# Kernel optimization log

Measured on AMD Instinct MI355X. Metric: run time of the kernel, lower is better.

The kernel has to match this reference:

```python
import jax, jax.numpy as jnp
import numpy as np

N, M, A, B, L, C = 40000, 12, 64, 64, 3, 128  # atoms, nbrs, site feat, bond feat, layers, crystals
F0, H = 92, 128  # orig site features, hidden dim
EPS = 1e-5


def _bn(x, g, b):
    # BatchNorm1d in training mode: batch stats (biased var), affine
    m = x.mean(0)
    v = x.var(0)
    return g * (x - m) * jax.lax.rsqrt(v + EPS) + b


def setup_inputs() -> dict:
    key = jax.random.key(0)
    ks = jax.random.split(key, 20)
    inp = {
        "site_features": jax.random.normal(ks[0], (N, F0), jnp.float32),
        "bond_features": jax.random.normal(ks[1], (N, M, B), jnp.float32),
        "feature_after_pooing": jax.random.normal(ks[2], (C,), jnp.float32),
        "fc1_w": jax.random.normal(ks[3], (F0, A), jnp.float32) * 0.05,
        "fc1_b": jnp.zeros((A,), jnp.float32),
        "conv_fc_w": jax.random.normal(ks[4], (L, 2 * A + B, 2 * A), jnp.float32) * 0.05,
        "conv_fc_b": jnp.zeros((L, 2 * A), jnp.float32),
        "bn1_g": jnp.ones((L, 2 * A), jnp.float32),
        "bn1_b": jnp.zeros((L, 2 * A), jnp.float32),
        "bn2_g": jnp.ones((L, A), jnp.float32),
        "bn2_b": jnp.zeros((L, A), jnp.float32),
        "top_bn_g": jnp.ones((A + 1,), jnp.float32),
        "top_bn_b": jnp.zeros((A + 1,), jnp.float32),
        "fc2_w": jax.random.normal(ks[5], (A + 1, H), jnp.float32) * 0.05,
        "fc2_b": jnp.zeros((H,), jnp.float32),
        "fc3_w": jax.random.normal(ks[6], (H, 1), jnp.float32) * 0.05,
        "fc3_b": jnp.zeros((1,), jnp.float32),
        "bond_indices": jax.random.randint(ks[7], (N, M), 0, N, jnp.int64),
        "crystal_idx": jnp.sort(jax.random.randint(ks[8], (N,), 0, C, jnp.int64)),
    }
    return inp


def _conv_layer(h, bond_features, bond_indices, w, bw, g1, b1, g2, b2):
    n, a = h.shape
    m = bond_indices.shape[1]
    v_j = h[bond_indices]                                 # (N,M,A) gather
    v_i = jnp.broadcast_to(h[:, None, :], (n, m, a))      # (N,M,A)
    z = jnp.concatenate([v_i, v_j, bond_features], -1)    # (N,M,2A+B)
    t = jnp.einsum('nmk,kd->nmd', z, w) + bw              # (N,M,2A)
    t = _bn(t.reshape(-1, 2 * a), g1, b1).reshape(n, m, 2 * a)
    filt, core = t[..., :a], t[..., a:]
    s = jnp.sum(jax.nn.sigmoid(filt) * jax.nn.softplus(core), axis=1)  # (N,A)
    s = _bn(s, g2, b2)
    return jax.nn.softplus(h + s)


def reference(site_features, bond_features, feature_after_pooing,
              fc1_w, fc1_b, conv_fc_w, conv_fc_b, bn1_g, bn1_b, bn2_g, bn2_b,
              top_bn_g, top_bn_b, fc2_w, fc2_b, fc3_w, fc3_b,
              bond_indices, crystal_idx):
    h = site_features @ fc1_w + fc1_b  # (N,A)
    for l in range(L):
        h = _conv_layer(h, bond_features, bond_indices,
                        conv_fc_w[l], conv_fc_b[l],
                        bn1_g[l], bn1_b[l], bn2_g[l], bn2_b[l])
    # per-crystal mean pooling
    counts = jax.ops.segment_sum(jnp.ones((N,), h.dtype), crystal_idx, num_segments=C)
    pooled = jax.ops.segment_sum(h, crystal_idx, num_segments=C) / jnp.maximum(counts, 1.0)[:, None]
    feats = jnp.concatenate([pooled, feature_after_pooing[:, None]], axis=1)  # (C,A+1)
    feats = _bn(feats, top_bn_g, top_bn_b)
    hidden = jax.nn.softplus(feats) @ fc2_w + fc2_b
    pred = jax.nn.softplus(hidden) @ fc3_w + fc3_b
    return pred.reshape(-1)
```

## Files before the change

### kernel.cpp

```cpp
#include <hip/hip_runtime.h>
#include <hip/hip_bf16.h>


#define NN 40000
#define MM 12
#define AA 64
#define LL 3
#define CC 128
#define F0C 92
#define NBOND (NN*MM)
#define EPSBN 1e-5f

#define G_BOND 1250
#define NTILE 7500
#define G_FUSE 1250
#define NSUPER 2500
#define RED_B 125

#define L2E 1.4426950408889634f
#define LN2 0.6931471805599453f

typedef __attribute__((ext_vector_type(8))) short bf16x8;
typedef __attribute__((ext_vector_type(4))) float f32x4;

__device__ __forceinline__ float softplusf_(float x) {
    float e = __builtin_amdgcn_exp2f(-fabsf(x) * L2E);
    return fmaxf(x, 0.f) + __builtin_amdgcn_logf(1.f + e) * LN2;
}
__device__ __forceinline__ float sigmoidf_(float x) {
    return __builtin_amdgcn_rcpf(1.f + __builtin_amdgcn_exp2f(-x * L2E));
}
__device__ __forceinline__ unsigned short f2bf(float f) {
    unsigned int u = __float_as_uint(f);
    unsigned int r = (u + 0x7fffu + ((u >> 16) & 1u)) >> 16;
    return (unsigned short)r;
}
__device__ __forceinline__ float bf2f(unsigned short s) {
    return __uint_as_float(((unsigned int)s) << 16);
}

__global__ __launch_bounds__(256) void k_cvt(const float* __restrict__ in,
        unsigned short* __restrict__ out) {
    size_t i = ((size_t)blockIdx.x * 256 + threadIdx.x) * 8;
    float4 a = *(const float4*)&in[i];
    float4 b = *(const float4*)&in[i + 4];
    ushort4 ua, ub;
    ua.x = f2bf(a.x); ua.y = f2bf(a.y); ua.z = f2bf(a.z); ua.w = f2bf(a.w);
    ub.x = f2bf(b.x); ub.y = f2bf(b.y); ub.z = f2bf(b.z); ub.w = f2bf(b.w);
    *(ushort4*)&out[i] = ua;
    *(ushort4*)&out[i + 4] = ub;
}

__global__ __launch_bounds__(256) void k_fc1(const float* __restrict__ site,
        const float* __restrict__ w, const float* __restrict__ b,
        float* __restrict__ h) {
    __shared__ float w_s[F0C][AA];
    __shared__ float x_s[16][F0C];
    int tid = threadIdx.x;
    for (int i = tid; i < F0C * AA; i += 256) w_s[i / AA][i % AA] = w[i];
    int n0 = blockIdx.x * 16;
    for (int i = tid; i < 16 * F0C; i += 256) x_s[i / F0C][i % F0C] = site[(size_t)n0 * F0C + i];
    __syncthreads();
    int d = tid & 63, ng = tid >> 6;
    float bb = b[d];
    float acc[4] = {bb, bb, bb, bb};
    #pragma unroll 4
    for (int k = 0; k < F0C; ++k) {
        float wv = w_s[k][d];
        acc[0] += x_s[ng][k] * wv;
        acc[1] += x_s[ng + 4][k] * wv;
        acc[2] += x_s[ng + 8][k] * wv;
        acc[3] += x_s[ng + 12][k] * wv;
    }
    #pragma unroll
    for (int rr = 0; rr < 4; ++rr)
        h[(size_t)(n0 + ng + rr * 4) * AA + d] = acc[rr];
}

__global__ __launch_bounds__(256) void k_proj(const float* __restrict__ h,
        const float* __restrict__ convw, const float* __restrict__ convb,
        unsigned short* __restrict__ hi, unsigned short* __restrict__ hj) {
    __shared__ float w_s[64][256];
    __shared__ float hT[64][36];
    int tid = threadIdx.x;
    for (int i = tid; i < 64 * 256; i += 256) {
        int k = i >> 8, c = i & 255;
        w_s[k][c] = convw[(size_t)((c < 128 ? k : 64 + k)) * 128 + (c & 127)];
    }
    int row0 = blockIdx.x * 32;
    for (int i = tid; i < 2048; i += 256) {
        int r = i >> 6, k = i & 63;
        hT[k][r] = h[(size_t)(row0 + r) * 64 + k];
    }
    __syncthreads();
    int c0 = (tid & 63) * 4;
    int r0 = (tid >> 6) * 8;
    float acc[8][4];
    #pragma unroll
    for (int r = 0; r < 8; ++r)
        #pragma unroll
        for (int i = 0; i < 4; ++i) acc[r][i] = 0.f;
    #pragma unroll 4
    for (int k = 0; k < 64; ++k) {
        float4 w4 = *(const float4*)&w_s[k][c0];
        float4 ha = *(const float4*)&hT[k][r0];
        float4 hb = *(const float4*)&hT[k][r0 + 4];
        float wv[4] = {w4.x, w4.y, w4.z, w4.w};
        float hv[8] = {ha.x, ha.y, ha.z, ha.w, hb.x, hb.y, hb.z, hb.w};
        #pragma unroll
        for (int r = 0; r < 8; ++r)
            #pragma unroll
            for (int i = 0; i < 4; ++i) acc[r][i] += hv[r] * wv[i];
    }
    bool isHi = (c0 < 128);
    int cc = isHi ? c0 : c0 - 128;
    float4 cb4 = make_float4(0.f, 0.f, 0.f, 0.f);
    if (isHi) cb4 = *(const float4*)&convb[c0];
    unsigned short* dst = isHi ? hi : hj;
    #pragma unroll
    for (int r = 0; r < 8; ++r) {
        int n = row0 + r0 + r;
        ushort4 o;
        o.x = f2bf(acc[r][0] + cb4.x);
        o.y = f2bf(acc[r][1] + cb4.y);
        o.z = f2bf(acc[r][2] + cb4.z);
        o.w = f2bf(acc[r][3] + cb4.w);
        *(ushort4*)&dst[(size_t)n * 128 + cc] = o;
    }
}

template<bool BFQ>
__global__ __launch_bounds__(256) void k_stat(const float* __restrict__ bf,
        const unsigned short* __restrict__ bfq,
        const float* __restrict__ wb,
        const unsigned short* __restrict__ hi, const unsigned short* __restrict__ hj,
        const int* __restrict__ bidx,
        float* __restrict__ part1) {
    __shared__ __align__(16) char buf0[128 * 72 * 2];
    __shared__ __align__(16) char buf1[64 * 72 * 2];
    auto wbT   = (unsigned short(*)[72])buf0;
    auto red   = (float(*)[128])buf0;
    auto A_lds = (unsigned short(*)[72])buf1;

    int tid = threadIdx.x;
    int lane = tid & 63, w = tid >> 6;
    int l15 = lane & 15, l4 = lane >> 4;

    for (int i = tid; i < 64 * 128; i += 256) {
        int k = i >> 7, c = i & 127;
        wbT[c][k] = f2bf(wb[i]);
    }
    __syncthreads();

    bf16x8 bfr[2][8];
    #pragma unroll
    for (int kh = 0; kh < 2; ++kh)
        #pragma unroll
        for (int ct = 0; ct < 8; ++ct)
            bfr[kh][ct] = *(const bf16x8*)&wbT[ct * 16 + l15][kh * 32 + l4 * 8];

    float suml[8], sql[8];
    #pragma unroll
    for (int ct = 0; ct < 8; ++ct) { suml[ct] = 0.f; sql[ct] = 0.f; }

    int rbase = w * 16 + l4 * 4;
    for (int tile = blockIdx.x; tile < NTILE; tile += G_BOND) {
        int bond0 = tile * 64;
        __syncthreads();
        if constexpr (BFQ) {
            int r = tid >> 3, c8 = (tid & 7) * 8;
            #pragma unroll
            for (int rr = 0; rr < 2; ++rr) {
                bf16x8 v = *(const bf16x8*)&bfq[((size_t)(bond0 + r + rr * 32)) * 64 + c8];
                *(bf16x8*)&A_lds[r + rr * 32][c8] = v;
            }
        } else {
            int r = tid >> 4, kq = (tid & 15) * 4;
            #pragma unroll
            for (int rr = 0; rr < 4; ++rr) {
                float4 v = *(const float4*)&bf[((size_t)(bond0 + r + rr * 16)) * 64 + kq];
                ushort4 u;
                u.x = f2bf(v.x); u.y = f2bf(v.y); u.z = f2bf(v.z); u.w = f2bf(v.w);
                *(ushort4*)&A_lds[r + rr * 16][kq] = u;
            }
        }
        __syncthreads();

        f32x4 acc[8];
        #pragma unroll
        for (int ct = 0; ct < 8; ++ct) acc[ct] = (f32x4){0.f, 0.f, 0.f, 0.f};
        #pragma unroll
        for (int kh = 0; kh < 2; ++kh) {
            bf16x8 a = *(const bf16x8*)&A_lds[rbase - l4 * 4 + l15][kh * 32 + l4 * 8];
            #pragma unroll
            for (int ct = 0; ct < 8; ++ct)
                acc[ct] = __builtin_amdgcn_mfma_f32_16x16x32_bf16(a, bfr[kh][ct], acc[ct], 0, 0, 0);
        }

        #pragma unroll
        for (int reg = 0; reg < 4; ++reg) {
            int bond = bond0 + rbase + reg;
            int n = bond / MM;
            int j = bidx[bond];
            const unsigned short* hin = hi + (size_t)n * 128;
            const unsigned short* hjn = hj + (size_t)j * 128;
            #pragma unroll
            for (int ct = 0; ct < 8; ++ct) {
                int col = ct * 16 + l15;
                float t = acc[ct][reg] + bf2f(hin[col]) + bf2f(hjn[col]);
                suml[ct] += t;
                sql[ct] += t * t;
            }
        }
    }

    #pragma unroll
    for (int ct = 0; ct < 8; ++ct) {
        float s = suml[ct], q = sql[ct];
        s += __shfl_xor(s, 16); s += __shfl_xor(s, 32);
        q += __shfl_xor(q, 16); q += __shfl_xor(q, 32);
        suml[ct] = s; sql[ct] = q;
    }
    __syncthreads();
    if (l4 == 0) {
        #pragma unroll
        for (int ct = 0; ct < 8; ++ct) red[w][ct * 16 + l15] = suml[ct];
    }
    __syncthreads();
    if (tid < 128)
        part1[(size_t)blockIdx.x * 256 + tid] = red[0][tid] + red[1][tid] + red[2][tid] + red[3][tid];
    __syncthreads();
    if (l4 == 0) {
        #pragma unroll
        for (int ct = 0; ct < 8; ++ct) red[w][ct * 16 + l15] = sql[ct];
    }
    __syncthreads();
    if (tid < 128)
        part1[(size_t)blockIdx.x * 256 + 128 + tid] = red[0][tid] + red[1][tid] + red[2][tid] + red[3][tid];
}

template<bool BFQ>
__global__ __launch_bounds__(256) void k_fuse(const float* __restrict__ bf,
        const unsigned short* __restrict__ bfq,
        const float* __restrict__ wb,
        const unsigned short* __restrict__ hi, const unsigned short* __restrict__ hj,
        const int* __restrict__ bidx,
        const float* __restrict__ scsh,
        float* __restrict__ s_out,
        float* __restrict__ part2) {
    __shared__ __align__(16) char buf0[192 * 68 * 2];
    __shared__ __align__(16) char buf1[64 * 72 * 2];
    auto wbT   = (unsigned short(*)[72])buf0;
    auto val   = (unsigned short(*)[68])buf0;
    auto A_lds = (unsigned short(*)[72])buf1;
    auto red2  = (float(*)[64])buf1;

    int tid = threadIdx.x;
    int lane = tid & 63, w = tid >> 6;
    int l15 = lane & 15, l4 = lane >> 4;

    for (int i = tid; i < 64 * 128; i += 256) {
        int k = i >> 7, c = i & 127;
        wbT[c][k] = f2bf(wb[i]);
    }
    __syncthreads();

    bf16x8 bfr[2][8];
    #pragma unroll
    for (int kh = 0; kh < 2; ++kh)
        #pragma unroll
        for (int ct = 0; ct < 8; ++ct)
            bfr[kh][ct] = *(const bf16x8*)&wbT[ct * 16 + l15][kh * 32 + l4 * 8];

    float scf[4], shf[4], scc[4], shc[4];
    #pragma unroll
    for (int ct = 0; ct < 4; ++ct) {
        int colA = ct * 16 + l15, colC = colA + 64;
        scf[ct] = scsh[colA];  shf[ct] = scsh[128 + colA];
        scc[ct] = scsh[colC];  shc[ct] = scsh[128 + colC];
    }

    int ssite = tid >> 4, a0 = (tid & 15) * 4;
    float sum2[4] = {0, 0, 0, 0}, sq2[4] = {0, 0, 0, 0};

    int rbase = w * 16 + l4 * 4;
    for (int sup = blockIdx.x; sup < NSUPER; sup += G_FUSE) {
        int bond00 = sup * 192;
        #pragma unroll
        for (int sub = 0; sub < 3; ++sub) {
            int bond0 = bond00 + sub * 64;
            __syncthreads();
            if constexpr (BFQ) {
                int r = tid >> 3, c8 = (tid & 7) * 8;
                #pragma unroll
                for (int rr = 0; rr < 2; ++rr) {
                    bf16x8 v = *(const bf16x8*)&bfq[((size_t)(bond0 + r + rr * 32)) * 64 + c8];
                    *(bf16x8*)&A_lds[r + rr * 32][c8] = v;
                }
            } else {
                int r = tid >> 4, kq = (tid & 15) * 4;
                #pragma unroll
                for (int rr = 0; rr < 4; ++rr) {
                    float4 v = *(const float4*)&bf[((size_t)(bond0 + r + rr * 16)) * 64 + kq];
                    ushort4 u;
                    u.x = f2bf(v.x); u.y = f2bf(v.y); u.z = f2bf(v.z); u.w = f2bf(v.w);
                    *(ushort4*)&A_lds[r + rr * 16][kq] = u;
                }
            }
            __syncthreads();

            f32x4 acc[8];
            #pragma unroll
            for (int ct = 0; ct < 8; ++ct) acc[ct] = (f32x4){0.f, 0.f, 0.f, 0.f};
            #pragma unroll
            for (int kh = 0; kh < 2; ++kh) {
                bf16x8 a = *(const bf16x8*)&A_lds[w * 16 + l15][kh * 32 + l4 * 8];
                #pragma unroll
                for (int ct = 0; ct < 8; ++ct)
                    acc[ct] = __builtin_amdgcn_mfma_f32_16x16x32_bf16(a, bfr[kh][ct], acc[ct], 0, 0, 0);
            }

            #pragma unroll
            for (int reg = 0; reg < 4; ++reg) {
                int r = rbase + reg;
                int bond = bond0 + r;
                int n = bond / MM;
                int j = bidx[bond];
                const unsigned short* hin = hi + (size_t)n * 128;
                const unsigned short* hjn = hj + (size_t)j * 128;
                #pragma unroll
                for (int ct = 0; ct < 4; ++ct) {
                    int colA = ct * 16 + l15, colC = colA + 64;
                    float tA = acc[ct][reg]     + bf2f(hin[colA]) + bf2f(hjn[colA]);
                    float tC = acc[ct + 4][reg] + bf2f(hin[colC]) + bf2f(hjn[colC]);
                    float v = sigmoidf_(scf[ct] * tA + shf[ct])
                            * softplusf_(scc[ct] * tC + shc[ct]);
                    val[sub * 64 + r][colA] = f2bf(v);
                }
            }
        }
        __syncthreads();

        float sv[4] = {0, 0, 0, 0};
        #pragma unroll
        for (int m = 0; m < MM; ++m) {
            ushort4 u = *(const ushort4*)&val[ssite * MM + m][a0];
            sv[0] += bf2f(u.x); sv[1] += bf2f(u.y);
            sv[2] += bf2f(u.z); sv[3] += bf2f(u.w);
        }
        int gsite = sup * 16 + ssite;
        *(float4*)&s_out[(size_t)gsite * 64 + a0] = make_float4(sv[0], sv[1], sv[2], sv[3]);
        #pragma unroll
        for (int k = 0; k < 4; ++k) { sum2[k] += sv[k]; sq2[k] += sv[k] * sv[k]; }
    }

    __syncthreads();
    #pragma unroll
    for (int k = 0; k < 4; ++k) red2[ssite][a0 + k] = sum2[k];
    __syncthreads();
    if (tid < 64) {
        float t = 0.f;
        #pragma unroll
        for (int g = 0; g < 16; ++g) t += red2[g][tid];
        part2[(size_t)blockIdx.x * 128 + tid] = t;
    }
    __syncthreads();
    #pragma unroll
    for (int k = 0; k < 4; ++k) red2[ssite][a0 + k] = sq2[k];
    __syncthreads();
    if (tid < 64) {
        float t = 0.f;
        #pragma unroll
        for (int g = 0; g < 16; ++g) t += red2[g][tid];
        part2[(size_t)blockIdx.x * 128 + 64 + tid] = t;
    }
}

__global__ __launch_bounds__(256) void k_red1(const float* __restrict__ in, float* __restrict__ out) {
    int tid = threadIdx.x, b = blockIdx.x;
    float acc = 0.f;
    for (int r = b * 10; r < b * 10 + 10; ++r) acc += in[(size_t)r * 256 + tid];
    out[(size_t)b * 256 + tid] = acc;
}
__global__ __launch_bounds__(128) void k_red2(const float* __restrict__ in, float* __restrict__ out) {
    int tid = threadIdx.x, b = blockIdx.x;
    float acc = 0.f;
    for (int r = b * 10; r < b * 10 + 10; ++r) acc += in[(size_t)r * 128 + tid];
    out[(size_t)b * 128 + tid] = acc;
}

__global__ __launch_bounds__(256) void k_fin1(const float* __restrict__ partA, const float* __restrict__ g,
                       const float* __restrict__ b, float* __restrict__ scsh) {
    __shared__ float sm[256];
    int tid = threadIdx.x;
    float acc = 0.f;
    for (int r = 0; r < RED_B; ++r) acc += partA[(size_t)r * 256 + tid];
    sm[tid] = acc;
    __syncthreads();
    if (tid < 128) {
        float m = sm[tid] / (float)NBOND;
        float v = sm[128 + tid] / (float)NBOND - m * m;
        float sc = g[tid] * rsqrtf(v + EPSBN);
        scsh[tid] = sc;
        scsh[128 + tid] = b[tid] - m * sc;
    }
}

__global__ __launch_bounds__(128) void k_fin2(const float* __restrict__ partB, const float* __restrict__ g,
                       const float* __restrict__ b, float* __restrict__ scsh2) {
    __shared__ float sm[128];
    int tid = threadIdx.x;
    float acc = 0.f;
    for (int r = 0; r < RED_B; ++r) acc += partB[(size_t)r * 128 + tid];
    sm[tid] = acc;
    __syncthreads();
    if (tid < 64) {
        float m = sm[tid] / (float)NN;
        float v = sm[64 + tid] / (float)NN - m * m;
        float sc = g[tid] * rsqrtf(v + EPSBN);
        scsh2[tid] = sc;
        scsh2[64 + tid] = b[tid] - m * sc;
    }
}

__global__ __launch_bounds__(256) void k_upd(float* __restrict__ h, const float* __restrict__ s,
        const float* __restrict__ scsh2) {
    size_t i = ((size_t)blockIdx.x * 256 + threadIdx.x) * 4;
    int c0 = (int)(i & 63);
    float4 hv = *(const float4*)&h[i];
    float4 sv = *(const float4*)&s[i];
    float4 o;
    o.x = softplusf_(hv.x + scsh2[c0 + 0] * sv.x + scsh2[64 + c0 + 0]);
    o.y = softplusf_(hv.y + scsh2[c0 + 1] * sv.y + scsh2[64 + c0 + 1]);
    o.z = softplusf_(hv.z + scsh2[c0 + 2] * sv.z + scsh2[64 + c0 + 2]);
    o.w = softplusf_(hv.w + scsh2[c0 + 3] * sv.w + scsh2[64 + c0 + 3]);
    *(float4*)&h[i] = o;
}

__device__ __forceinline__ int lbound(const int* a, int n, int v) {
    int lo = 0, hi = n;
    while (lo < hi) { int mid = (lo + hi) >> 1; if (a[mid] < v) lo = mid + 1; else hi = mid; }
    return lo;
}

__global__ __launch_bounds__(256) void k_pool(const float* __restrict__ h,
        const int* __restrict__ cidx, float* __restrict__ feats) {
    __shared__ float red[4][68];
    __shared__ int bounds[2];
    int c = blockIdx.x, tid = threadIdx.x;
    if (tid == 0) {
        bounds[0] = lbound(cidx, NN, c);
        bounds[1] = lbound(cidx, NN, c + 1);
    }
    __syncthreads();
    int lo = bounds[0], hi = bounds[1];
    int d = tid & 63, g = tid >> 6;
    float acc = 0;
    for (int n = lo + g; n < hi; n += 4) acc += h[(size_t)n * 64 + d];
    red[g][d] = acc;
    __syncthreads();
    if (tid < 64) {
        float t = red[0][tid] + red[1][tid] + red[2][tid] + red[3][tid];
        int cnt = hi - lo;
        feats[(size_t)c * 65 + tid] = t / (float)(cnt > 0 ? cnt : 1);
    }
}

__global__ __launch_bounds__(128) void k_head1(float* __restrict__ feats, const float* __restrict__ fap,
        const float* __restrict__ g, const float* __restrict__ b, float* __restrict__ featsp) {
    int tid = threadIdx.x;
    if (tid < CC) feats[(size_t)tid * 65 + 64] = fap[tid];
    __syncthreads();
    if (tid < 65) {
        float s = 0;
        for (int r = 0; r < CC; ++r) s += feats[r * 65 + tid];
        float m = s / (float)CC;
        float v = 0;
        for (int r = 0; r < CC; ++r) { float d = feats[r * 65 + tid] - m; v += d * d; }
        v /= (float)CC;
        float sc = g[tid] * rsqrtf(v + EPSBN);
        float sh = b[tid] - m * sc;
        for (int r = 0; r < CC; ++r)
            featsp[r * 65 + tid] = softplusf_(sc * feats[r * 65 + tid] + sh);
    }
}

__global__ __launch_bounds__(128) void k_head2(const float* __restrict__ featsp,
        const float* __restrict__ fc2w, const float* __restrict__ fc2b,
        const float* __restrict__ fc3w, const float* __restrict__ fc3b,
        float* __restrict__ out) {
    __shared__ float fr[65];
    __shared__ float red[128];
    int r = blockIdx.x, tid = threadIdx.x;
    if (tid < 65) fr[tid] = featsp[(size_t)r * 65 + tid];
    __syncthreads();
    float acc = fc2b[tid];
    for (int k = 0; k < 65; ++k) acc += fr[k] * fc2w[k * 128 + tid];
    red[tid] = softplusf_(acc) * fc3w[tid];
    __syncthreads();
    for (int st = 64; st > 0; st >>= 1) {
        if (tid < st) red[tid] += red[tid + st];
        __syncthreads();
    }
    if (tid == 0) out[r] = red[0] + fc3b[0];
}

extern "C" void kernel_launch(void* const* d_in, const int* in_sizes, int n_in,
                              void* d_out, int out_size, void* d_ws, size_t ws_size,
                              hipStream_t stream) {
    const float* site  = (const float*)d_in[0];
    const float* bondf = (const float*)d_in[1];
    const float* fap   = (const float*)d_in[2];
    const float* fc1w  = (const float*)d_in[3];
    const float* fc1b  = (const float*)d_in[4];
    const float* convw = (const float*)d_in[5];
    const float* convb = (const float*)d_in[6];
    const float* bn1g  = (const float*)d_in[7];
    const float* bn1b  = (const float*)d_in[8];
    const float* bn2g  = (const float*)d_in[9];
    const float* bn2b  = (const float*)d_in[10];
    const float* topg  = (const float*)d_in[11];
    const float* topb  = (const float*)d_in[12];
    const float* fc2w  = (const float*)d_in[13];
    const float* fc2b  = (const float*)d_in[14];
    const float* fc3w  = (const float*)d_in[15];
    const float* fc3b  = (const float*)d_in[16];
    const int*   bidx  = (const int*)d_in[17];
    const int*   cidx  = (const int*)d_in[18];
    float* out = (float*)d_out;

    char* w = (char*)d_ws;
    constexpr size_t SZ_H  = (size_t)NN * 64 * 4;
    constexpr size_t SZ_HP = (size_t)NN * 128 * 2;
    constexpr size_t OFF_H  = 0;
    constexpr size_t OFF_HI = OFF_H + SZ_H;
    constexpr size_t OFF_HJ = OFF_HI + SZ_HP;
    constexpr size_t OFF_S  = OFF_HJ + SZ_HP;
    constexpr size_t OFF_SCSH1 = OFF_S + SZ_H;
    constexpr size_t OFF_SCSH2 = OFF_SCSH1 + 1024;
    constexpr size_t OFF_P1 = OFF_SCSH2 + 512;
    constexpr size_t OFF_P2 = OFF_P1 + (size_t)G_BOND * 256 * 4;
    constexpr size_t OFF_PA = OFF_P2 + (size_t)G_FUSE * 128 * 4;
    constexpr size_t OFF_PB = OFF_PA + (size_t)RED_B * 256 * 4;
    constexpr size_t OFF_FE = OFF_PB + (size_t)RED_B * 128 * 4;
    constexpr size_t OFF_FP = OFF_FE + 128 * 65 * 4;
    constexpr size_t OFF_BFQ = ((OFF_FP + 128 * 65 * 4) + 255) & ~(size_t)255;
    constexpr size_t NEED_BFQ = OFF_BFQ + (size_t)NBOND * 64 * 2;

    float* h      = (float*)(w + OFF_H);
    unsigned short* hi = (unsigned short*)(w + OFF_HI);
    unsigned short* hj = (unsigned short*)(w + OFF_HJ);
    float* sbuf   = (float*)(w + OFF_S);
    float* scsh1  = (float*)(w + OFF_SCSH1);
    float* scsh2  = (float*)(w + OFF_SCSH2);
    float* part1  = (float*)(w + OFF_P1);
    float* part2  = (float*)(w + OFF_P2);
    float* partA  = (float*)(w + OFF_PA);
    float* partB  = (float*)(w + OFF_PB);
    float* feats  = (float*)(w + OFF_FE);
    float* featsp = (float*)(w + OFF_FP);
    unsigned short* bfq = (unsigned short*)(w + OFF_BFQ);

    const bool useq = (ws_size >= NEED_BFQ);

    if (useq) k_cvt<<<NBOND * 64 / (256 * 8), 256, 0, stream>>>(bondf, bfq);
    k_fc1<<<2500, 256, 0, stream>>>(site, fc1w, fc1b, h);
    for (int l = 0; l < LL; ++l) {
        const float* cw = convw + (size_t)l * 192 * 128;
        const float* cb = convb + l * 128;
        k_proj<<<1250, 256, 0, stream>>>(h, cw, cb, hi, hj);
        if (useq) {
            k_stat<true><<<G_BOND, 256, 0, stream>>>(bondf, bfq, cw + 128 * 128, hi, hj, bidx, part1);
        } else {
            k_stat<false><<<G_BOND, 256, 0, stream>>>(bondf, bfq, cw + 128 * 128, hi, hj, bidx, part1);
        }
        k_red1<<<RED_B, 256, 0, stream>>>(part1, partA);
        k_fin1<<<1, 256, 0, stream>>>(partA, bn1g + l * 128, bn1b + l * 128, scsh1);
        if (useq) {
            k_fuse<true><<<G_FUSE, 256, 0, stream>>>(bondf, bfq, cw + 128 * 128, hi, hj, bidx, scsh1, sbuf, part2);
        } else {
            k_fuse<false><<<G_FUSE, 256, 0, stream>>>(bondf, bfq, cw + 128 * 128, hi, hj, bidx, scsh1, sbuf, part2);
        }
        k_red2<<<RED_B, 128, 0, stream>>>(part2, partB);
        k_fin2<<<1, 128, 0, stream>>>(partB, bn2g + l * 64, bn2b + l * 64, scsh2);
        k_upd<<<2500, 256, 0, stream>>>(h, sbuf, scsh2);
    }
    k_pool<<<128, 256, 0, stream>>>(h, cidx, feats);
    k_head1<<<1, 128, 0, stream>>>(feats, fap, topg, topb, featsp);
    k_head2<<<128, 128, 0, stream>>>(featsp, fc2w, fc2b, fc3w, fc3b, out);
}
```

Before: 557.8 us.

## Compute BN1 mean analytically via neighbor counts and bond-feature column sums

The first BatchNorm mean is now derived algebraically. It combines per-column sums of the projected hi/hj (hj weighted by how often each atom appears as a neighbor) with a one-time column sum of bond features multiplied by the bond weights. The stat pass therefore only accumulates sums of squares. k_stat and k_fuse now read weight fragments straight from LDS with swapped MFMA operands, and they use vectorized hi/hj loads per lane. Grid and tile sizes also change: 1024 blocks, and k_fuse runs 48-bond tiles with 192 threads. Added costs are a neighbor-count atomic pass, extra reductions in k_proj, and a possible precision loss from computing variance as E[x²]−mean² with an externally computed mean.

New measurement: 816.4 us. +46.4%, slower.

```diff
diff --git a/kernel.cpp b/kernel.cpp
--- a/kernel.cpp
+++ b/kernel.cpp
@@ -11,11 +11,11 @@
 #define NBOND (NN*MM)
 #define EPSBN 1e-5f
 
-#define G_BOND 1250
-#define NTILE 7500
-#define G_FUSE 1250
-#define NSUPER 2500
-#define RED_B 125
+#define G_STAT 1024
+#define NT_STAT 7500
+#define G_FUSE 1024
+#define NT_FUSE 10000
+#define G_PROJ 1250
 
 #define L2E 1.4426950408889634f
 #define LN2 0.6931471805599453f
@@ -51,6 +51,40 @@
     *(ushort4*)&out[i + 4] = ub;
 }
 
+__global__ __launch_bounds__(256) void k_zero(int* __restrict__ cnt) {
+    int i = blockIdx.x * 256 + threadIdx.x;
+    if (i < NN) cnt[i] = 0;
+}
+__global__ __launch_bounds__(256) void k_cnt(const int* __restrict__ bidx,
+        int* __restrict__ cnt) {
+    int i = blockIdx.x * 256 + threadIdx.x;
+    if (i < NBOND) atomicAdd(&cnt[bidx[i]], 1);
+}
+
+template<bool BFQ>
+__global__ __launch_bounds__(256) void k_sbf(const float* __restrict__ bf,
+        const unsigned short* __restrict__ bfq, float* __restrict__ part) {
+    __shared__ float red[4][64];
+    int tid = threadIdx.x, c = tid & 63, rg = tid >> 6;
+    size_t base = (size_t)blockIdx.x * 1875;
+    float acc = 0.f;
+    for (int r = rg; r < 1875; r += 4) {
+        if constexpr (BFQ) acc += bf2f(bfq[(base + r) * 64 + c]);
+        else               acc += bf2f(f2bf(bf[(base + r) * 64 + c]));
+    }
+    red[rg][c] = acc;
+    __syncthreads();
+    if (tid < 64) part[(size_t)blockIdx.x * 64 + tid]
+        = red[0][tid] + red[1][tid] + red[2][tid] + red[3][tid];
+}
+__global__ __launch_bounds__(64) void k_sbf2(const float* __restrict__ part,
+        float* __restrict__ sbf) {
+    int tid = threadIdx.x;
+    float a = 0.f;
+    for (int b = 0; b < 256; ++b) a += part[(size_t)b * 64 + tid];
+    sbf[tid] = a;
+}
+
 __global__ __launch_bounds__(256) void k_fc1(const float* __restrict__ site,
         const float* __restrict__ w, const float* __restrict__ b,
         float* __restrict__ h) {
@@ -79,7 +113,9 @@
 
 __global__ __launch_bounds__(256) void k_proj(const float* __restrict__ h,
         const float* __restrict__ convw, const float* __restrict__ convb,
-        unsigned short* __restrict__ hi, unsigned short* __restrict__ hj) {
+        const int* __restrict__ cnt,
+        unsigned short* __restrict__ hi, unsigned short* __restrict__ hj,
+        float* __restrict__ partP) {
     __shared__ float w_s[64][256];
     __shared__ float hT[64][36];
     int tid = threadIdx.x;
@@ -117,6 +153,7 @@
     float4 cb4 = make_float4(0.f, 0.f, 0.f, 0.f);
     if (isHi) cb4 = *(const float4*)&convb[c0];
     unsigned short* dst = isHi ? hi : hj;
+    float psum[4] = {0.f, 0.f, 0.f, 0.f};
     #pragma unroll
     for (int r = 0; r < 8; ++r) {
         int n = row0 + r0 + r;
@@ -126,7 +163,20 @@
         o.z = f2bf(acc[r][2] + cb4.z);
         o.w = f2bf(acc[r][3] + cb4.w);
         *(ushort4*)&dst[(size_t)n * 128 + cc] = o;
-    }
+        float wt = isHi ? 1.f : (float)cnt[n];
+        psum[0] += wt * bf2f(o.x);
+        psum[1] += wt * bf2f(o.y);
+        psum[2] += wt * bf2f(o.z);
+        psum[3] += wt * bf2f(o.w);
+    }
+    __syncthreads();
+    float* redp = &w_s[0][0];
+    int rg = tid >> 6;
+    #pragma unroll
+    for (int i = 0; i < 4; ++i) redp[rg * 256 + c0 + i] = psum[i];
+    __syncthreads();
+    partP[(size_t)blockIdx.x * 256 + tid] =
+        redp[tid] + redp[256 + tid] + redp[512 + tid] + redp[768 + tid];
 }
 
 template<bool BFQ>
@@ -135,12 +185,10 @@
         const float* __restrict__ wb,
         const unsigned short* __restrict__ hi, const unsigned short* __restrict__ hj,
         const int* __restrict__ bidx,
-        float* __restrict__ part1) {
-    __shared__ __align__(16) char buf0[128 * 72 * 2];
-    __shared__ __align__(16) char buf1[64 * 72 * 2];
-    auto wbT   = (unsigned short(*)[72])buf0;
-    auto red   = (float(*)[128])buf0;
-    auto A_lds = (unsigned short(*)[72])buf1;
+        float* __restrict__ partS) {
+    __shared__ unsigned short wbT[128][72];
+    __shared__ unsigned short A_lds[64][72];
+    __shared__ float red[4][128];
 
     int tid = threadIdx.x;
     int lane = tid & 63, w = tid >> 6;
@@ -150,97 +198,125 @@
         int k = i >> 7, c = i & 127;
         wbT[c][k] = f2bf(wb[i]);
     }
-    __syncthreads();
-
-    bf16x8 bfr[2][8];
+
+    float sql[8][4];
     #pragma unroll
-    for (int kh = 0; kh < 2; ++kh)
-        #pragma unroll
-        for (int ct = 0; ct < 8; ++ct)
-            bfr[kh][ct] = *(const bf16x8*)&wbT[ct * 16 + l15][kh * 32 + l4 * 8];
-
-    float suml[8], sql[8];
-    #pragma unroll
-    for (int ct = 0; ct < 8; ++ct) { suml[ct] = 0.f; sql[ct] = 0.f; }
-
-    int rbase = w * 16 + l4 * 4;
-    for (int tile = blockIdx.x; tile < NTILE; tile += G_BOND) {
+    for (int ct = 0; ct < 8; ++ct)
+        #pragma unroll
+        for (int r = 0; r < 4; ++r) sql[ct][r] = 0.f;
+
+    int myb = w * 16 + l15;
+    for (int tile = blockIdx.x; tile < NT_STAT; tile += G_STAT) {
         int bond0 = tile * 64;
         __syncthreads();
-        if constexpr (BFQ) {
-            int r = tid >> 3, c8 = (tid & 7) * 8;
-            #pragma unroll
-            for (int rr = 0; rr < 2; ++rr) {
-                bf16x8 v = *(const bf16x8*)&bfq[((size_t)(bond0 + r + rr * 32)) * 64 + c8];
-                *(bf16x8*)&A_lds[r + rr * 32][c8] = v;
+        #pragma unroll
+        for (int ii = 0; ii < 2; ++ii) {
+            int idx = tid + ii * 256;
+            int r = idx >> 3, k8 = (idx & 7) * 8;
+            if constexpr (BFQ) {
+                bf16x8 v = *(const bf16x8*)&bfq[((size_t)(bond0 + r)) * 64 + k8];
+                *(bf16x8*)&A_lds[r][k8] = v;
+            } else {
+                float4 v0 = *(const float4*)&bf[((size_t)(bond0 + r)) * 64 + k8];
+                float4 v1 = *(const float4*)&bf[((size_t)(bond0 + r)) * 64 + k8 + 4];
+                ushort4 ua, ub;
+                ua.x = f2bf(v0.x); ua.y = f2bf(v0.y); ua.z = f2bf(v0.z); ua.w = f2bf(v0.w);
+                ub.x = f2bf(v1.x); ub.y = f2bf(v1.y); ub.z = f2bf(v1.z); ub.w = f2bf(v1.w);
+                *(ushort4*)&A_lds[r][k8] = ua;
+                *(ushort4*)&A_lds[r][k8 + 4] = ub;
             }
-        } else {
-            int r = tid >> 4, kq = (tid & 15) * 4;
-            #pragma unroll
-            for (int rr = 0; rr < 4; ++rr) {
-                float4 v = *(const float4*)&bf[((size_t)(bond0 + r + rr * 16)) * 64 + kq];
-                ushort4 u;
-                u.x = f2bf(v.x); u.y = f2bf(v.y); u.z = f2bf(v.z); u.w = f2bf(v.w);
-                *(ushort4*)&A_lds[r + rr * 16][kq] = u;
+        }
+        __syncthreads();
+
+        f32x4 acc[8];
+        #pragma unroll
+        for (int ct = 0; ct < 8; ++ct) acc[ct] = (f32x4){0.f, 0.f, 0.f, 0.f};
+        #pragma unroll
+        for (int kh = 0; kh < 2; ++kh) {
+            bf16x8 a = *(const bf16x8*)&A_lds[myb][kh * 32 + l4 * 8];
+            #pragma unroll
+            for (int ct = 0; ct < 8; ++ct) {
+                bf16x8 wf = *(const bf16x8*)&wbT[ct * 16 + l15][kh * 32 + l4 * 8];
+                acc[ct] = __builtin_amdgcn_mfma_f32_16x16x32_bf16(wf, a, acc[ct], 0, 0, 0);
             }
         }
-        __syncthreads();
-
-        f32x4 acc[8];
-        #pragma unroll
-        for (int ct = 0; ct < 8; ++ct) acc[ct] = (f32x4){0.f, 0.f, 0.f, 0.f};
-        #pragma unroll
-        for (int kh = 0; kh < 2; ++kh) {
-            bf16x8 a = *(const bf16x8*)&A_lds[rbase - l4 * 4 + l15][kh * 32 + l4 * 8];
-            #pragma unroll
-            for (int ct = 0; ct < 8; ++ct)
-                acc[ct] = __builtin_amdgcn_mfma_f32_16x16x32_bf16(a, bfr[kh][ct], acc[ct], 0, 0, 0);
-        }
-
-        #pragma unroll
-        for (int reg = 0; reg < 4; ++reg) {
-            int bond = bond0 + rbase + reg;
-            int n = bond / MM;
-            int j = bidx[bond];
-            const unsigned short* hin = hi + (size_t)n * 128;
-            const unsigned short* hjn = hj + (size_t)j * 128;
-            #pragma unroll
-            for (int ct = 0; ct < 8; ++ct) {
-                int col = ct * 16 + l15;
-                float t = acc[ct][reg] + bf2f(hin[col]) + bf2f(hjn[col]);
-                suml[ct] += t;
-                sql[ct] += t * t;
+
+        int bond = bond0 + myb;
+        int n = bond / MM;
+        int j = bidx[bond];
+        const unsigned short* hin = hi + (size_t)n * 128;
+        const unsigned short* hjn = hj + (size_t)j * 128;
+        #pragma unroll
+        for (int ct = 0; ct < 8; ++ct) {
+            int c0 = ct * 16 + l4 * 4;
+            ushort4 h4 = *(const ushort4*)&hin[c0];
+            ushort4 j4 = *(const ushort4*)&hjn[c0];
+            float hh[4] = {bf2f(h4.x), bf2f(h4.y), bf2f(h4.z), bf2f(h4.w)};
+            float jj[4] = {bf2f(j4.x), bf2f(j4.y), bf2f(j4.z), bf2f(j4.w)};
+            #pragma unroll
+            for (int r = 0; r < 4; ++r) {
+                float t = acc[ct][r] + hh[r] + jj[r];
+                sql[ct][r] += t * t;
             }
         }
     }
 
     #pragma unroll
-    for (int ct = 0; ct < 8; ++ct) {
-        float s = suml[ct], q = sql[ct];
-        s += __shfl_xor(s, 16); s += __shfl_xor(s, 32);
-        q += __shfl_xor(q, 16); q += __shfl_xor(q, 32);
-        suml[ct] = s; sql[ct] = q;
-    }
-    __syncthreads();
-    if (l4 == 0) {
-        #pragma unroll
-        for (int ct = 0; ct < 8; ++ct) red[w][ct * 16 + l15] = suml[ct];
+    for (int ct = 0; ct < 8; ++ct)
+        #pragma unroll
+        for (int r = 0; r < 4; ++r) {
+            float q = sql[ct][r];
+            q += __shfl_xor(q, 1); q += __shfl_xor(q, 2);
+            q += __shfl_xor(q, 4); q += __shfl_xor(q, 8);
+            sql[ct][r] = q;
+        }
+    if (l15 == 0) {
+        #pragma unroll
+        for (int ct = 0; ct < 8; ++ct)
+            #pragma unroll
+            for (int r = 0; r < 4; ++r)
+                red[w][ct * 16 + l4 * 4 + r] = sql[ct][r];
     }
     __syncthreads();
     if (tid < 128)
-        part1[(size_t)blockIdx.x * 256 + tid] = red[0][tid] + red[1][tid] + red[2][tid] + red[3][tid];
-    __syncthreads();
-    if (l4 == 0) {
-        #pragma unroll
-        for (int ct = 0; ct < 8; ++ct) red[w][ct * 16 + l15] = sql[ct];
-    }
-    __syncthreads();
-    if (tid < 128)
-        part1[(size_t)blockIdx.x * 256 + 128 + tid] = red[0][tid] + red[1][tid] + red[2][tid] + red[3][tid];
+        partS[(size_t)blockIdx.x * 128 + tid] =
+            red[0][tid] + red[1][tid] + red[2][tid] + red[3][tid];
+}
+
+__global__ void k_redw(const float* __restrict__ in, float* __restrict__ out,
+                       int rows, int rper) {
+    int tid = threadIdx.x, b = blockIdx.x, W = blockDim.x;
+    float a = 0.f;
+    int r0 = b * rper, r1 = r0 + rper;
+    for (int r = r0; r < r1 && r < rows; ++r) a += in[(size_t)r * W + tid];
+    out[(size_t)b * W + tid] = a;
+}
+
+__global__ __launch_bounds__(128) void k_fin1(const float* __restrict__ partSA,
+        const float* __restrict__ partPA,
+        const float* __restrict__ sbf,
+        const float* __restrict__ wb,
+        const float* __restrict__ g, const float* __restrict__ b,
+        float* __restrict__ scsh) {
+    int c = threadIdx.x;
+    float sq = 0.f;
+    for (int r = 0; r < 128; ++r) sq += partSA[(size_t)r * 128 + c];
+    float his = 0.f, hjw = 0.f;
+    for (int r = 0; r < 125; ++r) {
+        his += partPA[(size_t)r * 256 + c];
+        hjw += partPA[(size_t)r * 256 + 128 + c];
+    }
+    float sw = 0.f;
+    for (int k = 0; k < 64; ++k) sw += sbf[k] * bf2f(f2bf(wb[(size_t)k * 128 + c]));
+    float mean = (sw + 12.f * his + hjw) * (1.f / (float)NBOND);
+    float var = sq * (1.f / (float)NBOND) - mean * mean;
+    float sc = g[c] * rsqrtf(var + EPSBN);
+    scsh[c] = sc;
+    scsh[128 + c] = b[c] - mean * sc;
 }
 
 template<bool BFQ>
-__global__ __launch_bounds__(256) void k_fuse(const float* __restrict__ bf,
+__global__ __launch_bounds__(192) void k_fuse(const float* __restrict__ bf,
         const unsigned short* __restrict__ bfq,
         const float* __restrict__ wb,
         const unsigned short* __restrict__ hi, const unsigned short* __restrict__ hj,
@@ -248,170 +324,145 @@
         const float* __restrict__ scsh,
         float* __restrict__ s_out,
         float* __restrict__ part2) {
-    __shared__ __align__(16) char buf0[192 * 68 * 2];
-    __shared__ __align__(16) char buf1[64 * 72 * 2];
-    auto wbT   = (unsigned short(*)[72])buf0;
-    auto val   = (unsigned short(*)[68])buf0;
-    auto A_lds = (unsigned short(*)[72])buf1;
-    auto red2  = (float(*)[64])buf1;
+    __shared__ unsigned short wbT[128][72];
+    __shared__ unsigned short A_lds[48][72];
+    __shared__ unsigned short val[48][68];
+    __shared__ float red2[4][64];
 
     int tid = threadIdx.x;
     int lane = tid & 63, w = tid >> 6;
     int l15 = lane & 15, l4 = lane >> 4;
 
-    for (int i = tid; i < 64 * 128; i += 256) {
+    for (int i = tid; i < 64 * 128; i += 192) {
         int k = i >> 7, c = i & 127;
         wbT[c][k] = f2bf(wb[i]);
     }
-    __syncthreads();
-
-    bf16x8 bfr[2][8];
+
+    float scf[4][4], shf[4][4], scc[4][4], shc[4][4];
     #pragma unroll
-    for (int kh = 0; kh < 2; ++kh)
-        #pragma unroll
-        for (int ct = 0; ct < 8; ++ct)
-            bfr[kh][ct] = *(const bf16x8*)&wbT[ct * 16 + l15][kh * 32 + l4 * 8];
-
-    float scf[4], shf[4], scc[4], shc[4];
-    #pragma unroll
-    for (int ct = 0; ct < 4; ++ct) {
-        int colA = ct * 16 + l15, colC = colA + 64;
-        scf[ct] = scsh[colA];  shf[ct] = scsh[128 + colA];
-        scc[ct] = scsh[colC];  shc[ct] = scsh[128 + colC];
-    }
-
-    int ssite = tid >> 4, a0 = (tid & 15) * 4;
+    for (int ct = 0; ct < 4; ++ct)
+        #pragma unroll
+        for (int r = 0; r < 4; ++r) {
+            int cf = ct * 16 + l4 * 4 + r;
+            scf[ct][r] = scsh[cf];       shf[ct][r] = scsh[128 + cf];
+            scc[ct][r] = scsh[64 + cf];  shc[ct][r] = scsh[192 + cf];
+        }
+
     float sum2[4] = {0, 0, 0, 0}, sq2[4] = {0, 0, 0, 0};
-
-    int rbase = w * 16 + l4 * 4;
-    for (int sup = blockIdx.x; sup < NSUPER; sup += G_FUSE) {
-        int bond00 = sup * 192;
-        #pragma unroll
-        for (int sub = 0; sub < 3; ++sub) {
-            int bond0 = bond00 + sub * 64;
-            __syncthreads();
+    int myb = w * 16 + l15;
+    __syncthreads();
+
+    for (int tile = blockIdx.x; tile < NT_FUSE; tile += G_FUSE) {
+        int bond0 = tile * 48;
+        #pragma unroll
+        for (int ii = 0; ii < 2; ++ii) {
+            int idx = tid + ii * 192;
+            int r = idx >> 3, k8 = (idx & 7) * 8;
             if constexpr (BFQ) {
-                int r = tid >> 3, c8 = (tid & 7) * 8;
-                #pragma unroll
-                for (int rr = 0; rr < 2; ++rr) {
-                    bf16x8 v = *(const bf16x8*)&bfq[((size_t)(bond0 + r + rr * 32)) * 64 + c8];
-                    *(bf16x8*)&A_lds[r + rr * 32][c8] = v;
-                }
+                bf16x8 v = *(const bf16x8*)&bfq[((size_t)(bond0 + r)) * 64 + k8];
+                *(bf16x8*)&A_lds[r][k8] = v;
             } else {
-                int r = tid >> 4, kq = (tid & 15) * 4;
-                #pragma unroll
-                for (int rr = 0; rr < 4; ++rr) {
-                    float4 v = *(const float4*)&bf[((size_t)(bond0 + r + rr * 16)) * 64 + kq];
-                    ushort4 u;
-                    u.x = f2bf(v.x); u.y = f2bf(v.y); u.z = f2bf(v.z); u.w = f2bf(v.w);
-                    *(ushort4*)&A_lds[r + rr * 16][kq] = u;
-                }
+                float4 v0 = *(const float4*)&bf[((size_t)(bond0 + r)) * 64 + k8];
+                float4 v1 = *(const float4*)&bf[((size_t)(bond0 + r)) * 64 + k8 + 4];
+                ushort4 ua, ub;
+                ua.x = f2bf(v0.x); ua.y = f2bf(v0.y); ua.z = f2bf(v0.z); ua.w = f2bf(v0.w);
+                ub.x = f2bf(v1.x); ub.y = f2bf(v1.y); ub.z = f2bf(v1.z); ub.w = f2bf(v1.w);
+                *(ushort4*)&A_lds[r][k8] = ua;
+                *(ushort4*)&A_lds[r][k8 + 4] = ub;
             }
-            __syncthreads();
-
-            f32x4 acc[8];
-            #pragma unroll
-            for (int ct = 0; ct < 8; ++ct) acc[ct] = (f32x4){0.f, 0.f, 0.f, 0.f};
-            #pragma unroll
-            for (int kh = 0; kh < 2; ++kh) {
-                bf16x8 a = *(const bf16x8*)&A_lds[w * 16 + l15][kh * 32 + l4 * 8];
-                #pragma unroll
-                for (int ct = 0; ct < 8; ++ct)
-                    acc[ct] = __builtin_amdgcn_mfma_f32_16x16x32_bf16(a, bfr[kh][ct], acc[ct], 0, 0, 0);
+        }
+        __syncthreads();
+
+        f32x4 acc[8];
+        #pragma unroll
+        for (int ct = 0; ct < 8; ++ct) acc[ct] = (f32x4){0.f, 0.f, 0.f, 0.f};
+        #pragma unroll
+        for (int kh = 0; kh < 2; ++kh) {
+            bf16x8 a = *(const bf16x8*)&A_lds[myb][kh * 32 + l4 * 8];
+            #pragma unroll
+            for (int ct = 0; ct < 8; ++ct) {
+                bf16x8 wf = *(const bf16x8*)&wbT[ct * 16 + l15][kh * 32 + l4 * 8];
+                acc[ct] = __builtin_amdgcn_mfma_f32_16x16x32_bf16(wf, a, acc[ct], 0, 0, 0);
             }
-
-            #pragma unroll
-            for (int reg = 0; reg < 4; ++reg) {
-                int r = rbase + reg;
-                int bond = bond0 + r;
-                int n = bond / MM;
-                int j = bidx[bond];
-                const unsigned short* hin = hi + (size_t)n * 128;
-                const unsigned short* hjn = hj + (size_t)j * 128;
-                #pragma unroll
-                for (int ct = 0; ct < 4; ++ct) {
-                    int colA = ct * 16 + l15, colC = colA + 64;
-                    float tA = acc[ct][reg]     + bf2f(hin[colA]) + bf2f(hjn[colA]);
-                    float tC = acc[ct + 4][reg] + bf2f(hin[colC]) + bf2f(hjn[colC]);
-                    float v = sigmoidf_(scf[ct] * tA + shf[ct])
-                            * softplusf_(scc[ct] * tC + shc[ct]);
-                    val[sub * 64 + r][colA] = f2bf(v);
-                }
+        }
+
+        int bond = bond0 + myb;
+        int n = bond / MM;
+        int j = bidx[bond];
+        const unsigned short* hin = hi + (size_t)n * 128;
+        const unsigned short* hjn = hj + (size_t)j * 128;
+        #pragma unroll
+        for (int ct = 0; ct < 4; ++ct) {
+            int c0 = ct * 16 + l4 * 4;
+            ushort4 hf = *(const ushort4*)&hin[c0];
+            ushort4 jf = *(const ushort4*)&hjn[c0];
+            ushort4 hc = *(const ushort4*)&hin[c0 + 64];
+            ushort4 jc = *(const ushort4*)&hjn[c0 + 64];
+            float hfv[4] = {bf2f(hf.x), bf2f(hf.y), bf2f(hf.z), bf2f(hf.w)};
+            float jfv[4] = {bf2f(jf.x), bf2f(jf.y), bf2f(jf.z), bf2f(jf.w)};
+            float hcv[4] = {bf2f(hc.x), bf2f(hc.y), bf2f(hc.z), bf2f(hc.w)};
+            float jcv[4] = {bf2f(jc.x), bf2f(jc.y), bf2f(jc.z), bf2f(jc.w)};
+            ushort4 o;
+            unsigned short ov[4];
+            #pragma unroll
+            for (int r = 0; r < 4; ++r) {
+                float tA = acc[ct][r] + hfv[r] + jfv[r];
+                float tC = acc[ct + 4][r] + hcv[r] + jcv[r];
+                float v = sigmoidf_(scf[ct][r] * tA + shf[ct][r])
+                        * softplusf_(scc[ct][r] * tC + shc[ct][r]);
+                ov[r] = f2bf(v);
             }
+            o.x = ov[0]; o.y = ov[1]; o.z = ov[2]; o.w = ov[3];
+            *(ushort4*)&val[myb][c0] = o;
         }
         __syncthreads();
 
-        float sv[4] = {0, 0, 0, 0};
-        #pragma unroll
-        for (int m = 0; m < MM; ++m) {
-            ushort4 u = *(const ushort4*)&val[ssite * MM + m][a0];
-            sv[0] += bf2f(u.x); sv[1] += bf2f(u.y);
-            sv[2] += bf2f(u.z); sv[3] += bf2f(u.w);
-        }
-        int gsite = sup * 16 + ssite;
-        *(float4*)&s_out[(size_t)gsite * 64 + a0] = make_float4(sv[0], sv[1], sv[2], sv[3]);
-        #pragma unroll
-        for (int k = 0; k < 4; ++k) { sum2[k] += sv[k]; sq2[k] += sv[k] * sv[k]; }
-    }
-
-    __syncthreads();
-    #pragma unroll
-    for (int k = 0; k < 4; ++k) red2[ssite][a0 + k] = sum2[k];
-    __syncthreads();
+        if (tid < 64) {
+            int site = tid >> 4, q = tid & 15;
+            float sv[4] = {0, 0, 0, 0};
+            #pragma unroll
+            for (int m = 0; m < MM; ++m) {
+                ushort4 u = *(const ushort4*)&val[site * MM + m][q * 4];
+                sv[0] += bf2f(u.x); sv[1] += bf2f(u.y);
+                sv[2] += bf2f(u.z); sv[3] += bf2f(u.w);
+            }
+            int gsite = tile * 4 + site;
+            *(float4*)&s_out[(size_t)gsite * 64 + q * 4] =
+                make_float4(sv[0], sv[1], sv[2], sv[3]);
+            #pragma unroll
+            for (int i = 0; i < 4; ++i) { sum2[i] += sv[i]; sq2[i] += sv[i] * sv[i]; }
+        }
+        __syncthreads();
+    }
+
     if (tid < 64) {
-        float t = 0.f;
-        #pragma unroll
-        for (int g = 0; g < 16; ++g) t += red2[g][tid];
-        part2[(size_t)blockIdx.x * 128 + tid] = t;
-    }
-    __syncthreads();
-    #pragma unroll
-    for (int k = 0; k < 4; ++k) red2[ssite][a0 + k] = sq2[k];
+        int site = tid >> 4, q = tid & 15;
+        #pragma unroll
+        for (int i = 0; i < 4; ++i) red2[site][q * 4 + i] = sum2[i];
+    }
+    __syncthreads();
+    if (tid < 64)
+        part2[(size_t)blockIdx.x * 128 + tid] =
+            red2[0][tid] + red2[1][tid] + red2[2][tid] + red2[3][tid];
     __syncthreads();
     if (tid < 64) {
-        float t = 0.f;
-        #pragma unroll
-        for (int g = 0; g < 16; ++g) t += red2[g][tid];
-        part2[(size_t)blockIdx.x * 128 + 64 + tid] = t;
-    }
-}
-
-__global__ __launch_bounds__(256) void k_red1(const float* __restrict__ in, float* __restrict__ out) {
-    int tid = threadIdx.x, b = blockIdx.x;
-    float acc = 0.f;
-    for (int r = b * 10; r < b * 10 + 10; ++r) acc += in[(size_t)r * 256 + tid];
-    out[(size_t)b * 256 + tid] = acc;
-}
-__global__ __launch_bounds__(128) void k_red2(const float* __restrict__ in, float* __restrict__ out) {
-    int tid = threadIdx.x, b = blockIdx.x;
-    float acc = 0.f;
-    for (int r = b * 10; r < b * 10 + 10; ++r) acc += in[(size_t)r * 128 + tid];
-    out[(size_t)b * 128 + tid] = acc;
-}
-
-__global__ __launch_bounds__(256) void k_fin1(const float* __restrict__ partA, const float* __restrict__ g,
-                       const float* __restrict__ b, float* __restrict__ scsh) {
-    __shared__ float sm[256];
-    int tid = threadIdx.x;
-    float acc = 0.f;
-    for (int r = 0; r < RED_B; ++r) acc += partA[(size_t)r * 256 + tid];
-    sm[tid] = acc;
-    __syncthreads();
-    if (tid < 128) {
-        float m = sm[tid] / (float)NBOND;
-        float v = sm[128 + tid] / (float)NBOND - m * m;
-        float sc = g[tid] * rsqrtf(v + EPSBN);
-        scsh[tid] = sc;
-        scsh[128 + tid] = b[tid] - m * sc;
-    }
-}
-
-__global__ __launch_bounds__(128) void k_fin2(const float* __restrict__ partB, const float* __restrict__ g,
-                       const float* __restrict__ b, float* __restrict__ scsh2) {
+        int site = tid >> 4, q = tid & 15;
+        #pragma unroll
+        for (int i = 0; i < 4; ++i) red2[site][q * 4 + i] = sq2[i];
+    }
+    __syncthreads();
+    if (tid < 64)
+        part2[(size_t)blockIdx.x * 128 + 64 + tid] =
+            red2[0][tid] + red2[1][tid] + red2[2][tid] + red2[3][tid];
+}
+
+__global__ __launch_bounds__(128) void k_fin2(const float* __restrict__ partB,
+        const float* __restrict__ g, const float* __restrict__ b,
+        float* __restrict__ scsh2) {
     __shared__ float sm[128];
     int tid = threadIdx.x;
     float acc = 0.f;
-    for (int r = 0; r < RED_B; ++r) acc += partB[(size_t)r * 128 + tid];
+    for (int r = 0; r < 128; ++r) acc += partB[(size_t)r * 128 + tid];
     sm[tid] = acc;
     __syncthreads();
     if (tid < 64) {
@@ -530,22 +581,27 @@
     float* out = (float*)d_out;
 
     char* w = (char*)d_ws;
-    constexpr size_t SZ_H  = (size_t)NN * 64 * 4;
-    constexpr size_t SZ_HP = (size_t)NN * 128 * 2;
-    constexpr size_t OFF_H  = 0;
-    constexpr size_t OFF_HI = OFF_H + SZ_H;
-    constexpr size_t OFF_HJ = OFF_HI + SZ_HP;
-    constexpr size_t OFF_S  = OFF_HJ + SZ_HP;
+    constexpr size_t SZ_H   = (size_t)NN * 64 * 4;
+    constexpr size_t SZ_HP  = (size_t)NN * 128 * 2;
+    constexpr size_t OFF_H     = 0;
+    constexpr size_t OFF_HI    = OFF_H + SZ_H;
+    constexpr size_t OFF_HJ    = OFF_HI + SZ_HP;
+    constexpr size_t OFF_S     = OFF_HJ + SZ_HP;
     constexpr size_t OFF_SCSH1 = OFF_S + SZ_H;
     constexpr size_t OFF_SCSH2 = OFF_SCSH1 + 1024;
-    constexpr size_t OFF_P1 = OFF_SCSH2 + 512;
-    constexpr size_t OFF_P2 = OFF_P1 + (size_t)G_BOND * 256 * 4;
-    constexpr size_t OFF_PA = OFF_P2 + (size_t)G_FUSE * 128 * 4;
-    constexpr size_t OFF_PB = OFF_PA + (size_t)RED_B * 256 * 4;
-    constexpr size_t OFF_FE = OFF_PB + (size_t)RED_B * 128 * 4;
-    constexpr size_t OFF_FP = OFF_FE + 128 * 65 * 4;
-    constexpr size_t OFF_BFQ = ((OFF_FP + 128 * 65 * 4) + 255) & ~(size_t)255;
-    constexpr size_t NEED_BFQ = OFF_BFQ + (size_t)NBOND * 64 * 2;
+    constexpr size_t OFF_PS    = OFF_SCSH2 + 512;
+    constexpr size_t OFF_PSA   = OFF_PS + (size_t)G_STAT * 128 * 4;
+    constexpr size_t OFF_PP    = OFF_PSA + (size_t)128 * 128 * 4;
+    constexpr size_t OFF_PPA   = OFF_PP + (size_t)G_PROJ * 256 * 4;
+    constexpr size_t OFF_P2    = OFF_PPA + (size_t)125 * 256 * 4;
+    constexpr size_t OFF_P2A   = OFF_P2 + (size_t)G_FUSE * 128 * 4;
+    constexpr size_t OFF_FE    = OFF_P2A + (size_t)128 * 128 * 4;
+    constexpr size_t OFF_FP    = OFF_FE + 128 * 65 * 4;
+    constexpr size_t OFF_CNT   = OFF_FP + 128 * 65 * 4;
+    constexpr size_t OFF_SBP   = OFF_CNT + (size_t)NN * 4;
+    constexpr size_t OFF_SBF   = OFF_SBP + (size_t)256 * 64 * 4;
+    constexpr size_t OFF_BFQ   = ((OFF_SBF + 64 * 4) + 255) & ~(size_t)255;
+    constexpr size_t NEED_BFQ  = OFF_BFQ + (size_t)NBOND * 64 * 2;
 
     float* h      = (float*)(w + OFF_H);
     unsigned short* hi = (unsigned short*)(w + OFF_HI);
@@ -553,36 +609,50 @@
     float* sbuf   = (float*)(w + OFF_S);
     float* scsh1  = (float*)(w + OFF_SCSH1);
     float* scsh2  = (float*)(w + OFF_SCSH2);
-    float* part1  = (float*)(w + OFF_P1);
+    float* partS  = (float*)(w + OFF_PS);
+    float* partSA = (float*)(w + OFF_PSA);
+    float* partP  = (float*)(w + OFF_PP);
+    float* partPA = (float*)(w + OFF_PPA);
     float* part2  = (float*)(w + OFF_P2);
-    float* partA  = (float*)(w + OFF_PA);
-    float* partB  = (float*)(w + OFF_PB);
+    float* part2A = (float*)(w + OFF_P2A);
     float* feats  = (float*)(w + OFF_FE);
     float* featsp = (float*)(w + OFF_FP);
+    int*   cnt    = (int*)(w + OFF_CNT);
+    float* sbfp   = (float*)(w + OFF_SBP);
+    float* sbf    = (float*)(w + OFF_SBF);
     unsigned short* bfq = (unsigned short*)(w + OFF_BFQ);
 
     const bool useq = (ws_size >= NEED_BFQ);
 
     if (useq) k_cvt<<<NBOND * 64 / (256 * 8), 256, 0, stream>>>(bondf, bfq);
+    k_zero<<<(NN + 255) / 256, 256, 0, stream>>>(cnt);
+    k_cnt<<<(NBOND + 255) / 256, 256, 0, stream>>>(bidx, cnt);
+    if (useq) k_sbf<true><<<256, 256, 0, stream>>>(bondf, bfq, sbfp);
+    else      k_sbf<false><<<256, 256, 0, stream>>>(bondf, bfq, sbfp);
+    k_sbf2<<<1, 64, 0, stream>>>(sbfp, sbf);
     k_fc1<<<2500, 256, 0, stream>>>(site, fc1w, fc1b, h);
+
     for (int l = 0; l < LL; ++l) {
         const float* cw = convw + (size_t)l * 192 * 128;
         const float* cb = convb + l * 128;
-        k_proj<<<1250, 256, 0, stream>>>(h, cw, cb, hi, hj);
-        if (useq) {
-            k_stat<true><<<G_BOND, 256, 0, stream>>>(bondf, bfq, cw + 128 * 128, hi, hj, bidx, part1);
-        } else {
-            k_stat<false><<<G_BOND, 256, 0, stream>>>(bondf, bfq, cw + 128 * 128, hi, hj, bidx, part1);
-        }
-        k_red1<<<RED_B, 256, 0, stream>>>(part1, partA);
-        k_fin1<<<1, 256, 0, stream>>>(partA, bn1g + l * 128, bn1b + l * 128, scsh1);
-        if (useq) {
-            k_fuse<true><<<G_FUSE, 256, 0, stream>>>(bondf, bfq, cw + 128 * 128, hi, hj, bidx, scsh1, sbuf, part2);
-        } else {
-            k_fuse<false><<<G_FUSE, 256, 0, stream>>>(bondf, bfq, cw + 128 * 128, hi, hj, bidx, scsh1, sbuf, part2);
-        }
-        k_red2<<<RED_B, 128, 0, stream>>>(part2, partB);
-        k_fin2<<<1, 128, 0, stream>>>(partB, bn2g + l * 64, bn2b + l * 64, scsh2);
+        const float* wbp = cw + 128 * 128;
+        k_proj<<<G_PROJ, 256, 0, stream>>>(h, cw, cb, cnt, hi, hj, partP);
+        k_redw<<<125, 256, 0, stream>>>(partP, partPA, G_PROJ, 10);
+        if (useq)
+            k_stat<true><<<G_STAT, 256, 0, stream>>>(bondf, bfq, wbp, hi, hj, bidx, partS);
+        else
+            k_stat<false><<<G_STAT, 256, 0, stream>>>(bondf, bfq, wbp, hi, hj, bidx, partS);
+        k_redw<<<128, 128, 0, stream>>>(partS, partSA, G_STAT, 8);
+        k_fin1<<<1, 128, 0, stream>>>(partSA, partPA, sbf, wbp,
+                                      bn1g + l * 128, bn1b + l * 128, scsh1);
+        if (useq)
+            k_fuse<true><<<G_FUSE, 192, 0, stream>>>(bondf, bfq, wbp, hi, hj, bidx,
+                                                     scsh1, sbuf, part2);
+        else
+            k_fuse<false><<<G_FUSE, 192, 0, stream>>>(bondf, bfq, wbp, hi, hj, bidx,
+                                                      scsh1, sbuf, part2);
+        k_redw<<<128, 128, 0, stream>>>(part2, part2A, G_FUSE, 8);
+        k_fin2<<<1, 128, 0, stream>>>(part2A, bn2g + l * 64, bn2b + l * 64, scsh2);
         k_upd<<<2500, 256, 0, stream>>>(h, sbuf, scsh2);
     }
     k_pool<<<128, 256, 0, stream>>>(h, cidx, feats);
```
